# Optimization experiments

Measured on AMD Instinct MI355X. Metric: run time of the kernel, lower is better.

Reference implementation:

```python
import jax, jax.numpy as jnp
import numpy as np

D_STATE = 16


def setup_inputs() -> dict:
    key = jax.random.key(0)
    ks = jax.random.split(key, 7)
    B, S, D = 8, 4096, 64
    ds = D_STATE
    x = jax.random.normal(ks[0], (B, S, D), dtype=jnp.float32)
    # Selection layers modeled as Linear(d_model, out). W_A scaled small so the
    # random transition matrices are contractive over 4096 steps.
    W_A = jax.random.normal(ks[1], (D, ds * ds), dtype=jnp.float32) * 0.01
    b_A = jnp.zeros((ds * ds,), dtype=jnp.float32)
    W_B = jax.random.normal(ks[2], (D, ds * D), dtype=jnp.float32) * 0.05
    b_B = jnp.zeros((ds * D,), dtype=jnp.float32)
    W_C = jax.random.normal(ks[3], (D, ds * D), dtype=jnp.float32) * 0.05
    b_C = jnp.zeros((ds * D,), dtype=jnp.float32)
    return {"x": x, "W_A": W_A, "b_A": b_A, "W_B": W_B, "b_B": b_B,
            "W_C": W_C, "b_C": b_C}


def reference(x, W_A, b_A, W_B, b_B, W_C, b_C):
    B, S, D = x.shape
    ds = D_STATE
    # Input-dependent (selective) parameters per timestep
    A = (x @ W_A + b_A).reshape(B, S, ds, ds)      # [B,S,ds,ds]
    Bm = (x @ W_B + b_B).reshape(B, S, ds, D)      # [B,S,ds,D]
    Cm = (x @ W_C + b_C).reshape(B, S, ds, D)      # [B,S,ds,D]
    # Pre-contract B_t @ x_t once: [B,S,ds]
    Bx = jnp.einsum('bsnd,bsd->bsn', Bm, x)

    def step(h, inputs):
        A_t, Bx_t = inputs                          # [B,ds,ds], [B,ds]
        h = jnp.einsum('bij,bj->bi', A_t, h) + Bx_t
        return h, h

    h0 = jnp.zeros((B, ds), dtype=x.dtype)
    _, hs = jax.lax.scan(step, h0,
                         (jnp.swapaxes(A, 0, 1), jnp.swapaxes(Bx, 0, 1)))
    hs = jnp.swapaxes(hs, 0, 1)                     # [B,S,ds]
    # output_t = C_t^T @ h_t  -> [B,S,D]
    return jnp.einsum('bsnd,bsn->bsd', Cm, hs)
```

## Files before the change

### kernel.cpp

```cpp
#include <hip/hip_runtime.h>

#define BATCH   8
#define SEQ     4096
#define DM      64
#define DS      16
#define BS      (BATCH*SEQ)
#define CHUNK   16
#define NCHT    (BS/CHUNK)
#define SG      16
#define NSG     (NCHT/SG)

typedef __attribute__((ext_vector_type(8))) __bf16 bf16x8;
typedef __attribute__((ext_vector_type(4))) float  f32x4;

__device__ __forceinline__ unsigned short f2bf(float f) {
  unsigned int u = __float_as_uint(f);
  u += 0x7fffu + ((u >> 16) & 1u);
  return (unsigned short)(u >> 16);
}
__device__ __forceinline__ float bflo(unsigned int u) { return __uint_as_float(u << 16); }
__device__ __forceinline__ float bfhi(unsigned int u) { return __uint_as_float(u & 0xffff0000u); }

#define AS_I 20
#define AS_T 324

__global__ __launch_bounds__(256) void k0_castw(
    const float* __restrict__ WA, const float* __restrict__ WB,
    const float* __restrict__ WC,
    unsigned short* __restrict__ WBApk, unsigned short* __restrict__ WCpk)
{
  const int o = blockIdx.x * 256 + threadIdx.x;
  if (o < 81920) {
    int idx = o;
    const int e = idx & 7;    idx >>= 3;
    const int f = idx % 10;   idx /= 10;
    const int quad = idx & 3; idx >>= 2;
    const int l15 = idx & 15; idx >>= 4;
    const int n = idx;
    float src;
    if (f < 8) {
      const int r = f >> 1, h = f & 1;
      src = WB[(h * 32 + quad * 8 + e) * 1024 + (n * 4 + r) * 16 + l15];
    } else {
      const int h = f - 8;
      src = WA[(h * 32 + quad * 8 + e) * 256 + n * 16 + l15];
    }
    WBApk[o] = f2bf(src);
  } else {
    const int p = o - 81920;
    const int e = p & 7;
    const int h = (p >> 3) & 1;
    const int quad = (p >> 4) & 3;
    const int l15 = (p >> 6) & 15;
    const int nr = p >> 10;
    WCpk[p] = f2bf(WC[(h * 32 + quad * 8 + e) * 1024 + nr * 16 + l15]);
  }
}

struct WFrag {
  bf16x8 b00, b01, b10, b11, b20, b21, b30, b31;
  bf16x8 a0f, a1f;
  float  ba;
};

__device__ __forceinline__ WFrag loadw(
    const unsigned short* __restrict__ WBApk,
    const float* __restrict__ bA, int n, int l15, int quad)
{
  WFrag f;
  const bf16x8* fp = (const bf16x8*)(WBApk + (size_t)((n * 16 + l15) * 4 + quad) * 80);
  f.b00 = fp[0]; f.b01 = fp[1];
  f.b10 = fp[2]; f.b11 = fp[3];
  f.b20 = fp[4]; f.b21 = fp[5];
  f.b30 = fp[6]; f.b31 = fp[7];
  f.a0f = fp[8]; f.a1f = fp[9];
  f.ba  = bA[n * 16 + l15];
  return f;
}

__global__ __launch_bounds__(256, 4) void g1a(
    const float* __restrict__ x, const unsigned short* __restrict__ WBApk,
    const float* __restrict__ bB, const float* __restrict__ bA,
    unsigned short* __restrict__ xb, unsigned short* __restrict__ Wt_ws,
    float* __restrict__ u_ws)
{
  __shared__ __align__(16) float xs[32][68];
  __shared__ __align__(16) float bBs[1024];
  __shared__ __align__(16) unsigned short As[32 * AS_T];
  __shared__ __align__(16) float bxs[32][16];

  const int tid  = threadIdx.x;
  const int lane = tid & 63;
  const int l15  = lane & 15;
  const int quad = lane >> 4;
  const int w    = tid >> 6;
  const int tg   = w >> 1;
  const int nh   = w & 1;
  const int t0   = blockIdx.x * 32;
  const int twl  = tg * 16;
  const int n0   = nh * 8;

  {
    const float4* xg = (const float4*)(x + (size_t)t0 * DM);
    #pragma unroll
    for (int i = 0; i < 2; ++i) {
      const int f4 = tid + 256 * i;
      ((float4*)&xs[f4 >> 4][0])[f4 & 15] = xg[f4];
    }
    ((float4*)bBs)[tid] = ((const float4*)bB)[tid];
  }
  __syncthreads();

  WFrag cur = loadw(WBApk, bA, n0, l15, quad);

  bf16x8 a0, a1;
  {
    const int row = twl + l15;
    union { bf16x8 v; ushort4 s[2]; } ua, ub;
    float4 p0 = *(const float4*)&xs[row][quad * 8];
    float4 p1 = *(const float4*)&xs[row][quad * 8 + 4];
    float4 p2 = *(const float4*)&xs[row][32 + quad * 8];
    float4 p3 = *(const float4*)&xs[row][32 + quad * 8 + 4];
    ua.s[0] = (ushort4){f2bf(p0.x), f2bf(p0.y), f2bf(p0.z), f2bf(p0.w)};
    ua.s[1] = (ushort4){f2bf(p1.x), f2bf(p1.y), f2bf(p1.z), f2bf(p1.w)};
    ub.s[0] = (ushort4){f2bf(p2.x), f2bf(p2.y), f2bf(p2.z), f2bf(p2.w)};
    ub.s[1] = (ushort4){f2bf(p3.x), f2bf(p3.y), f2bf(p3.z), f2bf(p3.w)};
    a0 = ua.v; a1 = ub.v;
    if (nh == 0) {
      unsigned short* xp = xb + (size_t)(t0 + row) * 64 + quad * 8;
      *(bf16x8*)xp        = a0;
      *(bf16x8*)(xp + 32) = a1;
    }
  }

  float xv[4][4];
  #pragma unroll
  for (int r = 0; r < 4; ++r)
    #pragma unroll
    for (int reg = 0; reg < 4; ++reg)
      xv[r][reg] = xs[twl + quad * 4 + reg][r * 16 + l15];

  #pragma unroll
  for (int j = 0; j < 8; ++j) {
    const int n = n0 + j;
    WFrag nxt = (j < 7) ? loadw(WBApk, bA, n + 1, l15, quad) : cur;

    const f32x4 z4 = {0.f, 0.f, 0.f, 0.f};
    f32x4 aac = z4;
    aac = __builtin_amdgcn_mfma_f32_16x16x32_bf16(a0, cur.a0f, aac, 0, 0, 0);
    aac = __builtin_amdgcn_mfma_f32_16x16x32_bf16(a1, cur.a1f, aac, 0, 0, 0);

    f32x4 ac0 = z4, ac1 = z4, ac2 = z4, ac3 = z4;
    ac0 = __builtin_amdgcn_mfma_f32_16x16x32_bf16(a0, cur.b00, ac0, 0, 0, 0);
    ac0 = __builtin_amdgcn_mfma_f32_16x16x32_bf16(a1, cur.b01, ac0, 0, 0, 0);
    ac1 = __builtin_amdgcn_mfma_f32_16x16x32_bf16(a0, cur.b10, ac1, 0, 0, 0);
    ac1 = __builtin_amdgcn_mfma_f32_16x16x32_bf16(a1, cur.b11, ac1, 0, 0, 0);
    ac2 = __builtin_amdgcn_mfma_f32_16x16x32_bf16(a0, cur.b20, ac2, 0, 0, 0);
    ac2 = __builtin_amdgcn_mfma_f32_16x16x32_bf16(a1, cur.b21, ac2, 0, 0, 0);
    ac3 = __builtin_amdgcn_mfma_f32_16x16x32_bf16(a0, cur.b30, ac3, 0, 0, 0);
    ac3 = __builtin_amdgcn_mfma_f32_16x16x32_bf16(a1, cur.b31, ac3, 0, 0, 0);

    const float bb0 = bBs[n * 64 +  0 + l15];
    const float bb1 = bBs[n * 64 + 16 + l15];
    const float bb2 = bBs[n * 64 + 32 + l15];
    const float bb3 = bBs[n * 64 + 48 + l15];
    float part[4];
    #pragma unroll
    for (int reg = 0; reg < 4; ++reg) {
      float s = fmaf(ac0[reg] + bb0, xv[0][reg], 0.f);
      s = fmaf(ac1[reg] + bb1, xv[1][reg], s);
      s = fmaf(ac2[reg] + bb2, xv[2][reg], s);
      s = fmaf(ac3[reg] + bb3, xv[3][reg], s);
      part[reg] = s;
    }
    #pragma unroll
    for (int off = 1; off < 16; off <<= 1) {
      #pragma unroll
      for (int reg = 0; reg < 4; ++reg)
        part[reg] += __shfl_xor(part[reg], off, 64);
    }
    if (l15 == 0) {
      #pragma unroll
      for (int reg = 0; reg < 4; ++reg)
        bxs[twl + quad * 4 + reg][n] = part[reg];
    }

    As[(twl + quad * 4 + 0) * AS_T + n * AS_I + l15] = f2bf(aac[0] + cur.ba);
    As[(twl + quad * 4 + 1) * AS_T + n * AS_I + l15] = f2bf(aac[1] + cur.ba);
    As[(twl + quad * 4 + 2) * AS_T + n * AS_I + l15] = f2bf(aac[2] + cur.ba);
    As[(twl + quad * 4 + 3) * AS_T + n * AS_I + l15] = f2bf(aac[3] + cur.ba);

    cur = nxt;
  }
  __syncthreads();

  {
    uint4* Wg = (uint4*)(Wt_ws + (size_t)t0 * 256);
    #pragma unroll 1
    for (int z = 0; z < 4; ++z) {
      const int p4 = z * 256 + tid;
      const int f  = p4 * 8;
      const int t  = f >> 8, i = (f >> 4) & 15, k = f & 15;
      const unsigned short* sp = &As[t * AS_T + i * AS_I + k];
      uint2 lo = *(const uint2*)(sp);
      uint2 hi = *(const uint2*)(sp + 4);
      Wg[p4] = make_uint4(lo.x, lo.y, hi.x, hi.y);
    }
    if (tid < 128)
      ((float4*)(u_ws + (size_t)t0 * DS))[tid] = ((const float4*)&bxs[0][0])[tid];
  }
}

__global__ __launch_bounds__(256, 2) void g1b(
    unsigned short* __restrict__ Wt_ws, float* __restrict__ u_ws,
    float* __restrict__ P_ws, float* __restrict__ v_ws)
{
  __shared__ __align__(16) unsigned short As[64 * AS_T];
  __shared__ __align__(16) float bxs[64][16];
  __shared__ __align__(16) float us[4][16];

  const int tid  = threadIdx.x;
  const int lane = tid & 63;
  const int l15  = lane & 15;
  const int quad = lane >> 4;
  const int w    = tid >> 6;
  const int t0   = blockIdx.x * 64;
  const int twl  = w * 16;

  {
    const uint4* Wg = (const uint4*)(Wt_ws + (size_t)t0 * 256);
    #pragma unroll 1
    for (int z = 0; z < 8; ++z) {
      const int p4 = z * 256 + tid;
      const int f  = p4 * 8;
      const int t  = f >> 8, i = (f >> 4) & 15, k = f & 15;
      uint4 v = Wg[p4];
      unsigned short* sp = &As[t * AS_T + i * AS_I + k];
      *(uint2*)(sp)     = make_uint2(v.x, v.y);
      *(uint2*)(sp + 4) = make_uint2(v.z, v.w);
    }
    ((float4*)bxs)[tid] = ((const float4*)(u_ws + (size_t)t0 * DS))[tid];
    if (tid < 64) us[tid >> 4][tid & 15] = 0.f;
  }
  __syncthreads();

  {
    bf16x8 wb;
    #pragma unroll
    for (int j = 0; j < 8; ++j) wb[j] = (__bf16)((quad * 8 + j == l15) ? 1.f : 0.f);
    f32x4 d = {0.f, 0.f, 0.f, 0.f};
    const int qq = quad & 1;

    const unsigned short* rpp = &As[twl * AS_T + l15 * AS_I];
    uint2 r0 = *(const uint2*)(rpp);
    uint2 r1 = *(const uint2*)(rpp + 4);
    uint2 r2 = *(const uint2*)(rpp + 8);
    uint2 r3 = *(const uint2*)(rpp + 12);

    #pragma unroll 1
    for (int t = 0; t < CHUNK; ++t) {
      const int tl = twl + t;

      uint2 s0, s1, s2, s3;
      if (t < CHUNK - 1) {
        const unsigned short* rp = &As[(tl + 1) * AS_T + l15 * AS_I];
        s0 = *(const uint2*)(rp);
        s1 = *(const uint2*)(rp + 4);
        s2 = *(const uint2*)(rp + 8);
        s3 = *(const uint2*)(rp + 12);
      } else { s0 = r0; s1 = r1; s2 = r2; s3 = r3; }

      uint4 abits;
      if (quad == 0)      abits = make_uint4(r0.x, r0.y, r1.x, r1.y);
      else if (quad == 1) abits = make_uint4(r2.x, r2.y, r3.x, r3.y);
      else                abits = make_uint4(0u, 0u, 0u, 0u);
      bf16x8 af = *(bf16x8*)&abits;

      f32x4 z4 = {0.f, 0.f, 0.f, 0.f};
      d = __builtin_amdgcn_mfma_f32_16x16x32_bf16(af, wb, z4, 0, 0, 0);

      float nu;
      {
        float4 U0 = *(const float4*)&us[w][0];
        float4 U1 = *(const float4*)&us[w][4];
        float4 U2 = *(const float4*)&us[w][8];
        float4 U3 = *(const float4*)&us[w][12];
        float n0 = bxs[tl][l15], n1 = 0.f, n2 = 0.f, n3 = 0.f;
        n0 = fmaf(bflo(r0.x), U0.x, n0); n0 = fmaf(bfhi(r0.x), U0.y, n0);
        n0 = fmaf(bflo(r0.y), U0.z, n0); n0 = fmaf(bfhi(r0.y), U0.w, n0);
        n1 = fmaf(bflo(r1.x), U1.x, n1); n1 = fmaf(bfhi(r1.x), U1.y, n1);
        n1 = fmaf(bflo(r1.y), U1.z, n1); n1 = fmaf(bfhi(r1.y), U1.w, n1);
        n2 = fmaf(bflo(r2.x), U2.x, n2); n2 = fmaf(bfhi(r2.x), U2.y, n2);
        n2 = fmaf(bflo(r2.y), U2.z, n2); n2 = fmaf(bfhi(r2.y), U2.w, n2);
        n3 = fmaf(bflo(r3.x), U3.x, n3); n3 = fmaf(bfhi(r3.x), U3.y, n3);
        n3 = fmaf(bflo(r3.y), U3.z, n3); n3 = fmaf(bfhi(r3.y), U3.w, n3);
        nu = (n0 + n1) + (n2 + n3);
      }

      bf16x8 nb;
      nb[0] = (__bf16)__shfl(d[0], (2 * qq + 0) * 16 + l15, 64);
      nb[1] = (__bf16)__shfl(d[1], (2 * qq + 0) * 16 + l15, 64);
      nb[2] = (__bf16)__shfl(d[2], (2 * qq + 0) * 16 + l15, 64);
      nb[3] = (__bf16)__shfl(d[3], (2 * qq + 0) * 16 + l15, 64);
      nb[4] = (__bf16)__shfl(d[0], (2 * qq + 1) * 16 + l15, 64);
      nb[5] = (__bf16)__shfl(d[1], (2 * qq + 1) * 16 + l15, 64);
      nb[6] = (__bf16)__shfl(d[2], (2 * qq + 1) * 16 + l15, 64);
      nb[7] = (__bf16)__shfl(d[3], (2 * qq + 1) * 16 + l15, 64);
      wb = nb;

      if (quad == 0) {
        us[w][l15] = nu;
        bxs[tl][l15] = nu;
      }
      #pragma unroll
      for (int r = 0; r < 4; ++r)
        As[tl * AS_T + (quad * 4 + r) * AS_I + l15] = f2bf(d[r]);

      r0 = s0; r1 = s1; r2 = s2; r3 = s3;
    }

    const int chunk = blockIdx.x * 4 + w;
    #pragma unroll
    for (int r = 0; r < 4; ++r)
      P_ws[(size_t)chunk * 256 + (quad * 4 + r) * 16 + l15] = d[r];
    if (quad == 0) v_ws[(size_t)chunk * DS + l15] = us[w][l15];
  }
  __syncthreads();

  {
    uint4* Wg = (uint4*)(Wt_ws + (size_t)t0 * 256);
    #pragma unroll 1
    for (int z = 0; z < 8; ++z) {
      const int p4 = z * 256 + tid;
      const int f  = p4 * 8;
      const int t  = f >> 8, i = (f >> 4) & 15, k = f & 15;
      const unsigned short* sp = &As[t * AS_T + i * AS_I + k];
      uint2 lo = *(const uint2*)(sp);
      uint2 hi = *(const uint2*)(sp + 4);
      Wg[p4] = make_uint4(lo.x, lo.y, hi.x, hi.y);
    }
    ((float4*)(u_ws + (size_t)t0 * DS))[tid] = ((const float4*)&bxs[0][0])[tid];
  }
}

__global__ __launch_bounds__(1024, 4) void k3f(
    const float* __restrict__ P_ws, const float* __restrict__ v_ws,
    float* __restrict__ hb_ws,
    const unsigned short* __restrict__ Wt_ws,
    const unsigned short* __restrict__ xb,
    const float* __restrict__ u_ws)
{
  __shared__ float Qs[16][256];
  __shared__ float wsv[16][16];
  __shared__ float hbgs[16][16];

  const int tid = threadIdx.x;
  const int bx  = blockIdx.x;

  if (bx >= 8) {
    const uint4* wp = (const uint4*)(Wt_ws + (size_t)bx * 32 * 256);
    uint4 a = wp[tid];
    const unsigned int* xp = (const unsigned int*)(xb + (size_t)bx * 32 * 64);
    unsigned int b = xp[tid];
    unsigned int c = 0;
    if (tid < 512) c = ((const unsigned int*)(u_ws + (size_t)bx * 32 * DS))[tid];
    asm volatile("" :: "v"(a.x), "v"(b), "v"(c));
    return;
  }

  const int lane = tid & 63;
  const int l15  = lane & 15;
  const int quad = lane >> 4;
  const int wv   = tid >> 6;
  const int qq   = quad & 1;

  {
    const int s = bx * 16 + wv;
    if (lane < 16) wsv[wv][lane] = 0.f;
    bf16x8 wb;
    #pragma unroll
    for (int j = 0; j < 8; ++j) wb[j] = (__bf16)((quad * 8 + j == l15) ? 1.f : 0.f);
    f32x4 d = {0.f, 0.f, 0.f, 0.f};

    float4 p0 = {0.f,0.f,0.f,0.f}, p1 = {0.f,0.f,0.f,0.f};
    float nv;
    {
      const int chunk = s * SG;
      if (quad < 2) {
        const float4* pr = (const float4*)(P_ws + (size_t)chunk * 256 + l15 * 16 + quad * 8);
        p0 = pr[0]; p1 = pr[1];
      }
      nv = v_ws[(size_t)chunk * DS + l15];
    }

    #pragma unroll 1
    for (int t = 0; t < SG; ++t) {
      float4 q0 = {0.f,0.f,0.f,0.f}, q1 = {0.f,0.f,0.f,0.f};
      float nv2 = 0.f;
      if (t < SG - 1) {
        const int chunk = s * SG + t + 1;
        if (quad < 2) {
          const float4* pr = (const float4*)(P_ws + (size_t)chunk * 256 + l15 * 16 + quad * 8);
          q0 = pr[0]; q1 = pr[1];
        }
        nv2 = v_ws[(size_t)chunk * DS + l15];
      }

      bf16x8 af;
      af[0] = (__bf16)p0.x; af[1] = (__bf16)p0.y; af[2] = (__bf16)p0.z; af[3] = (__bf16)p0.w;
      af[4] = (__bf16)p1.x; af[5] = (__bf16)p1.y; af[6] = (__bf16)p1.z; af[7] = (__bf16)p1.w;

      f32x4 z4 = {0.f, 0.f, 0.f, 0.f};
      d = __builtin_amdgcn_mfma_f32_16x16x32_bf16(af, wb, z4, 0, 0, 0);

      float part = 0.f;
      if (quad < 2) {
        const float* wrow = &wsv[wv][quad * 8];
        part = p0.x*wrow[0] + p0.y*wrow[1] + p0.z*wrow[2] + p0.w*wrow[3]
             + p1.x*wrow[4] + p1.y*wrow[5] + p1.z*wrow[6] + p1.w*wrow[7];
      }
      part += __shfl_xor(part, 16, 64);

      bf16x8 nb;
      nb[0] = (__bf16)__shfl(d[0], (2 * qq + 0) * 16 + l15, 64);
      nb[1] = (__bf16)__shfl(d[1], (2 * qq + 0) * 16 + l15, 64);
      nb[2] = (__bf16)__shfl(d[2], (2 * qq + 0) * 16 + l15, 64);
      nb[3] = (__bf16)__shfl(d[3], (2 * qq + 0) * 16 + l15, 64);
      nb[4] = (__bf16)__shfl(d[0], (2 * qq + 1) * 16 + l15, 64);
      nb[5] = (__bf16)__shfl(d[1], (2 * qq + 1) * 16 + l15, 64);
      nb[6] = (__bf16)__shfl(d[2], (2 * qq + 1) * 16 + l15, 64);
      nb[7] = (__bf16)__shfl(d[3], (2 * qq + 1) * 16 + l15, 64);
      wb = nb;

      if (quad == 0) wsv[wv][l15] = part + nv;

      p0 = q0; p1 = q1; nv = nv2;
    }

    #pragma unroll
    for (int r = 0; r < 4; ++r)
      Qs[wv][(quad * 4 + r) * 16 + l15] = d[r];
  }
  __syncthreads();

  if (tid < 16) {
    const int r = tid;
    float h = 0.f;
    #pragma unroll 1
    for (int g = 0; g < 16; ++g) {
      hbgs[g][r] = h;
      const float4* Pr = (const float4*)&Qs[g][r * 16];
      float4 c0 = Pr[0], c1 = Pr[1], c2 = Pr[2], c3 = Pr[3];
      const float vc = wsv[g][r];
      float a0 = c0.x*__shfl(h, 0,16) + c0.y*__shfl(h, 1,16) + c0.z*__shfl(h, 2,16) + c0.w*__shfl(h, 3,16);
      float a1 = c1.x*__shfl(h, 4,16) + c1.y*__shfl(h, 5,16) + c1.z*__shfl(h, 6,16) + c1.w*__shfl(h, 7,16);
      float a2 = c2.x*__shfl(h, 8,16) + c2.y*__shfl(h, 9,16) + c2.z*__shfl(h,10,16) + c2.w*__shfl(h,11,16);
      float a3 = c3.x*__shfl(h,12,16) + c3.y*__shfl(h,13,16) + c3.z*__shfl(h,14,16) + c3.w*__shfl(h,15,16);
      h = vc + ((a0 + a1) + (a2 + a3));
    }
  }
  __syncthreads();

  if (tid < 256) {
    const int g = tid >> 4;
    const int r = tid & 15;
    const int s = bx * 16 + g;
    float h = hbgs[g][r];

    float4 c0, c1, c2, c3; float vc;
    {
      const int chunk = s * SG;
      const float4* Pr = (const float4*)&P_ws[(size_t)chunk * 256 + r * 16];
      c0 = Pr[0]; c1 = Pr[1]; c2 = Pr[2]; c3 = Pr[3];
      vc = v_ws[(size_t)chunk * DS + r];
    }

    #pragma unroll 1
    for (int t = 0; t < SG; ++t) {
      const int chunk = s * SG + t;
      float4 d0, d1, d2, d3; float vc2;
      if (t < SG - 1) {
        const float4* Pr = (const float4*)&P_ws[(size_t)(chunk + 1) * 256 + r * 16];
        d0 = Pr[0]; d1 = Pr[1]; d2 = Pr[2]; d3 = Pr[3];
        vc2 = v_ws[(size_t)(chunk + 1) * DS + r];
      } else { d0 = c0; d1 = c1; d2 = c2; d3 = c3; vc2 = vc; }

      hb_ws[(size_t)chunk * DS + r] = h;
      float a0 = c0.x*__shfl(h, 0,16) + c0.y*__shfl(h, 1,16) + c0.z*__shfl(h, 2,16) + c0.w*__shfl(h, 3,16);
      float a1 = c1.x*__shfl(h, 4,16) + c1.y*__shfl(h, 5,16) + c1.z*__shfl(h, 6,16) + c1.w*__shfl(h, 7,16);
      float a2 = c2.x*__shfl(h, 8,16) + c2.y*__shfl(h, 9,16) + c2.z*__shfl(h,10,16) + c2.w*__shfl(h,11,16);
      float a3 = c3.x*__shfl(h,12,16) + c3.y*__shfl(h,13,16) + c3.z*__shfl(h,14,16) + c3.w*__shfl(h,15,16);
      h = vc + ((a0 + a1) + (a2 + a3));

      c0 = d0; c1 = d1; c2 = d2; c3 = d3; vc = vc2;
    }
  }
}

__global__ __launch_bounds__(256, 8) void g2(
    const unsigned short* __restrict__ xb, const unsigned short* __restrict__ WCpk,
    const float* __restrict__ bC, const unsigned short* __restrict__ Wt_ws,
    const float* __restrict__ u_ws, const float* __restrict__ hb_ws,
    float* __restrict__ out)
{
  __shared__ float hsh[16][17];
  __shared__ float bCs[1024];
  const int tid  = threadIdx.x;
  const int lane = tid & 63;
  const int l15  = lane & 15;
  const int quad = lane >> 4;
  const int w    = tid >> 6;
  const int t0   = blockIdx.x * 16;
  const int rc   = w;

  ((float4*)bCs)[tid] = ((const float4*)bC)[tid];

  const bf16x8* xvp = (const bf16x8*)(xb + (size_t)(t0 + l15) * 64);
  bf16x8 a0 = xvp[quad];
  bf16x8 a1 = xvp[quad + 4];

  const int tl = tid >> 4, i = tid & 15;
  const int t  = t0 + tl;
  const uint4* wr = (const uint4*)(Wt_ws + (size_t)t * 256 + i * 16);
  uint4 wa = wr[0], wbv = wr[1];
  const float4* hp = (const float4*)(hb_ws + (size_t)blockIdx.x * DS);
  float4 h0 = hp[0], h1 = hp[1], h2 = hp[2], h3 = hp[3];
  float uu = u_ws[(size_t)t * DS + i];
  {
    float p0 = uu, p1 = 0.f, p2 = 0.f, p3 = 0.f;
    p0 = fmaf(bflo(wa.x),  h0.x, p0); p0 = fmaf(bfhi(wa.x),  h0.y, p0);
    p0 = fmaf(bflo(wa.y),  h0.z, p0); p0 = fmaf(bfhi(wa.y),  h0.w, p0);
    p1 = fmaf(bflo(wa.z),  h1.x, p1); p1 = fmaf(bfhi(wa.z),  h1.y, p1);
    p1 = fmaf(bflo(wa.w),  h1.z, p1); p1 = fmaf(bfhi(wa.w),  h1.w, p1);
    p2 = fmaf(bflo(wbv.x), h2.x, p2); p2 = fmaf(bfhi(wbv.x), h2.y, p2);
    p2 = fmaf(bflo(wbv.y), h2.z, p2); p2 = fmaf(bfhi(wbv.y), h2.w, p2);
    p3 = fmaf(bflo(wbv.z), h3.x, p3); p3 = fmaf(bfhi(wbv.z), h3.y, p3);
    p3 = fmaf(bflo(wbv.w), h3.z, p3); p3 = fmaf(bfhi(wbv.w), h3.w, p3);
    hsh[tl][i] = (p0 + p1) + (p2 + p3);
  }
  __syncthreads();

  f32x4 o0 = {0.f, 0.f, 0.f, 0.f};

  const bf16x8* cp = (const bf16x8*)(WCpk + (size_t)((0 * 4 + rc) * 64 + l15 * 4 + quad) * 16);
  bf16x8 c00 = cp[0], c01 = cp[1];
  #pragma unroll
  for (int n = 0; n < 16; ++n) {
    bf16x8 n00 = c00, n01 = c01;
    if (n < 15) {
      const bf16x8* np = (const bf16x8*)(WCpk + (size_t)(((n + 1) * 4 + rc) * 64 + l15 * 4 + quad) * 16);
      n00 = np[0]; n01 = np[1];
    }

    f32x4 ac0 = {0.f, 0.f, 0.f, 0.f};
    ac0 = __builtin_amdgcn_mfma_f32_16x16x32_bf16(a0, c00, ac0, 0, 0, 0);
    ac0 = __builtin_amdgcn_mfma_f32_16x16x32_bf16(a1, c01, ac0, 0, 0, 0);

    float hn[4];
    #pragma unroll
    for (int reg = 0; reg < 4; ++reg) hn[reg] = hsh[quad * 4 + reg][n];

    const float bc0 = bCs[n * 64 + rc * 16 + l15];
    #pragma unroll
    for (int reg = 0; reg < 4; ++reg)
      o0[reg] = fmaf(ac0[reg] + bc0, hn[reg], o0[reg]);

    c00 = n00; c01 = n01;
  }

  #pragma unroll
  for (int reg = 0; reg < 4; ++reg)
    out[(size_t)(t0 + quad * 4 + reg) * DM + rc * 16 + l15] = o0[reg];
}

extern "C" void kernel_launch(void* const* d_in, const int* in_sizes, int n_in,
                              void* d_out, int out_size, void* d_ws, size_t ws_size,
                              hipStream_t stream) {
  const float* x  = (const float*)d_in[0];
  const float* WA = (const float*)d_in[1];
  const float* bA = (const float*)d_in[2];
  const float* WB = (const float*)d_in[3];
  const float* bB = (const float*)d_in[4];
  const float* WC = (const float*)d_in[5];
  const float* bC = (const float*)d_in[6];
  float* out = (float*)d_out;

  float* ws     = (float*)d_ws;
  float* P_ws   = ws;
  float* v_ws   = P_ws   + (size_t)NCHT * 256;
  float* u_ws   = v_ws   + (size_t)NCHT * DS;
  float* Q_ws   = u_ws   + (size_t)BS * DS;
  float* w_ws   = Q_ws   + (size_t)NSG * 256;
  float* hbg_ws = w_ws   + (size_t)NSG * DS;
  float* hb_ws  = hbg_ws + (size_t)NSG * DS;
  unsigned short* xb    = (unsigned short*)(hb_ws + (size_t)NCHT * DS);
  unsigned short* WBApk = xb    + (size_t)BS * 64;
  unsigned short* WCpk  = WBApk + 81920;
  unsigned short* Wt_ws = WCpk  + 65536;

  k0_castw<<<576,      256, 0, stream>>>(WA, WB, WC, WBApk, WCpk);
  g1a     <<<BS / 32,  256, 0, stream>>>(x, WBApk, bB, bA, xb, Wt_ws, u_ws);
  g1b     <<<BS / 64,  256, 0, stream>>>(Wt_ws, u_ws, P_ws, v_ws);
  k3f     <<<1024,    1024, 0, stream>>>(P_ws, v_ws, hb_ws, Wt_ws, xb, u_ws);
  g2      <<<BS / 16,  256, 0, stream>>>(xb, WCpk, bC, Wt_ws, u_ws, hb_ws, out);
}
```

Measured before the change: 197.9 us.

## Fuse projection kernel g1a into chunk-scan kernel g1b to keep A in LDS

Merges the two phase-1 kernels into one block of 64 timesteps. Each wave now computes all 16 state rows of the A and Bx projections and leaves them in shared memory. This removes the separate launch and the global write and re-read of the packed A matrices and Bx between the two kernels. The cost is half as many waves on the projection stage, each with twice the serial MFMA work, and occupancy is capped at two blocks per CU. g2's launch bounds are also relaxed from 8 to 6 blocks per CU.

```diff
diff --git a/kernel.cpp b/kernel.cpp
--- a/kernel.cpp
+++ b/kernel.cpp
@@ -78,40 +78,40 @@
   return f;
 }
 
-__global__ __launch_bounds__(256, 4) void g1a(
+__global__ __launch_bounds__(256, 2) void g1(
     const float* __restrict__ x, const unsigned short* __restrict__ WBApk,
-    const float* __restrict__ bB, const float* __restrict__ bA,
-    unsigned short* __restrict__ xb, unsigned short* __restrict__ Wt_ws,
-    float* __restrict__ u_ws)
+    const float* __restrict__ bB,
+    const float* __restrict__ bA, unsigned short* __restrict__ xb,
+    unsigned short* __restrict__ Wt_ws, float* __restrict__ u_ws,
+    float* __restrict__ P_ws, float* __restrict__ v_ws)
 {
-  __shared__ __align__(16) float xs[32][68];
+  __shared__ __align__(16) float xs[64][68];
   __shared__ __align__(16) float bBs[1024];
-  __shared__ __align__(16) unsigned short As[32 * AS_T];
-  __shared__ __align__(16) float bxs[32][16];
+  __shared__ __align__(16) unsigned short As[64 * AS_T];
+  __shared__ __align__(16) float bxs[64][16];
+  __shared__ __align__(16) float us[4][16];
 
   const int tid  = threadIdx.x;
   const int lane = tid & 63;
   const int l15  = lane & 15;
   const int quad = lane >> 4;
   const int w    = tid >> 6;
-  const int tg   = w >> 1;
-  const int nh   = w & 1;
-  const int t0   = blockIdx.x * 32;
-  const int twl  = tg * 16;
-  const int n0   = nh * 8;
+  const int t0   = blockIdx.x * 64;
+  const int twl  = w * 16;
 
   {
     const float4* xg = (const float4*)(x + (size_t)t0 * DM);
     #pragma unroll
-    for (int i = 0; i < 2; ++i) {
+    for (int i = 0; i < 4; ++i) {
       const int f4 = tid + 256 * i;
       ((float4*)&xs[f4 >> 4][0])[f4 & 15] = xg[f4];
     }
     ((float4*)bBs)[tid] = ((const float4*)bB)[tid];
+    if (tid < 64) us[tid >> 4][tid & 15] = 0.f;
   }
   __syncthreads();
 
-  WFrag cur = loadw(WBApk, bA, n0, l15, quad);
+  WFrag cur = loadw(WBApk, bA, 0, l15, quad);
 
   bf16x8 a0, a1;
   {
@@ -126,11 +126,9 @@
     ub.s[0] = (ushort4){f2bf(p2.x), f2bf(p2.y), f2bf(p2.z), f2bf(p2.w)};
     ub.s[1] = (ushort4){f2bf(p3.x), f2bf(p3.y), f2bf(p3.z), f2bf(p3.w)};
     a0 = ua.v; a1 = ub.v;
-    if (nh == 0) {
-      unsigned short* xp = xb + (size_t)(t0 + row) * 64 + quad * 8;
-      *(bf16x8*)xp        = a0;
-      *(bf16x8*)(xp + 32) = a1;
-    }
+    unsigned short* xp = xb + (size_t)(t0 + row) * 64 + quad * 8;
+    *(bf16x8*)xp        = a0;
+    *(bf16x8*)(xp + 32) = a1;
   }
 
   float xv[4][4];
@@ -141,9 +139,8 @@
       xv[r][reg] = xs[twl + quad * 4 + reg][r * 16 + l15];
 
   #pragma unroll
-  for (int j = 0; j < 8; ++j) {
-    const int n = n0 + j;
-    WFrag nxt = (j < 7) ? loadw(WBApk, bA, n + 1, l15, quad) : cur;
+  for (int n = 0; n < 16; ++n) {
+    WFrag nxt = (n < 15) ? loadw(WBApk, bA, n + 1, l15, quad) : cur;
 
     const f32x4 z4 = {0.f, 0.f, 0.f, 0.f};
     f32x4 aac = z4;
@@ -192,57 +189,6 @@
 
     cur = nxt;
   }
-  __syncthreads();
-
-  {
-    uint4* Wg = (uint4*)(Wt_ws + (size_t)t0 * 256);
-    #pragma unroll 1
-    for (int z = 0; z < 4; ++z) {
-      const int p4 = z * 256 + tid;
-      const int f  = p4 * 8;
-      const int t  = f >> 8, i = (f >> 4) & 15, k = f & 15;
-      const unsigned short* sp = &As[t * AS_T + i * AS_I + k];
-      uint2 lo = *(const uint2*)(sp);
-      uint2 hi = *(const uint2*)(sp + 4);
-      Wg[p4] = make_uint4(lo.x, lo.y, hi.x, hi.y);
-    }
-    if (tid < 128)
-      ((float4*)(u_ws + (size_t)t0 * DS))[tid] = ((const float4*)&bxs[0][0])[tid];
-  }
-}
-
-__global__ __launch_bounds__(256, 2) void g1b(
-    unsigned short* __restrict__ Wt_ws, float* __restrict__ u_ws,
-    float* __restrict__ P_ws, float* __restrict__ v_ws)
-{
-  __shared__ __align__(16) unsigned short As[64 * AS_T];
-  __shared__ __align__(16) float bxs[64][16];
-  __shared__ __align__(16) float us[4][16];
-
-  const int tid  = threadIdx.x;
-  const int lane = tid & 63;
-  const int l15  = lane & 15;
-  const int quad = lane >> 4;
-  const int w    = tid >> 6;
-  const int t0   = blockIdx.x * 64;
-  const int twl  = w * 16;
-
-  {
-    const uint4* Wg = (const uint4*)(Wt_ws + (size_t)t0 * 256);
-    #pragma unroll 1
-    for (int z = 0; z < 8; ++z) {
-      const int p4 = z * 256 + tid;
-      const int f  = p4 * 8;
-      const int t  = f >> 8, i = (f >> 4) & 15, k = f & 15;
-      uint4 v = Wg[p4];
-      unsigned short* sp = &As[t * AS_T + i * AS_I + k];
-      *(uint2*)(sp)     = make_uint2(v.x, v.y);
-      *(uint2*)(sp + 4) = make_uint2(v.z, v.w);
-    }
-    ((float4*)bxs)[tid] = ((const float4*)(u_ws + (size_t)t0 * DS))[tid];
-    if (tid < 64) us[tid >> 4][tid & 15] = 0.f;
-  }
-  __syncthreads();
 
   {
     bf16x8 wb;
@@ -497,7 +443,7 @@
   }
 }
 
-__global__ __launch_bounds__(256, 8) void g2(
+__global__ __launch_bounds__(256, 6) void g2(
     const unsigned short* __restrict__ xb, const unsigned short* __restrict__ WCpk,
     const float* __restrict__ bC, const unsigned short* __restrict__ Wt_ws,
     const float* __restrict__ u_ws, const float* __restrict__ hb_ws,
@@ -599,8 +545,7 @@
   unsigned short* Wt_ws = WCpk  + 65536;
 
   k0_castw<<<576,      256, 0, stream>>>(WA, WB, WC, WBApk, WCpk);
-  g1a     <<<BS / 32,  256, 0, stream>>>(x, WBApk, bB, bA, xb, Wt_ws, u_ws);
-  g1b     <<<BS / 64,  256, 0, stream>>>(Wt_ws, u_ws, P_ws, v_ws);
+  g1      <<<BS / 64,  256, 0, stream>>>(x, WBApk, bB, bA, xb, Wt_ws, u_ws, P_ws, v_ws);
   k3f     <<<1024,    1024, 0, stream>>>(P_ws, v_ws, hb_ws, Wt_ws, xb, u_ws);
   g2      <<<BS / 16,  256, 0, stream>>>(xb, WCpk, bC, Wt_ws, u_ws, hb_ws, out);
 }
```

New measurement: 175.0 us. -11.6%, faster.
